# Kernel tuning notes

Hardware: AMD Instinct MI355X
Metric: run time of the kernel (lower is better)

The kernel has to match this reference:

```python
import jax, jax.numpy as jnp
import numpy as np
import math

N, L, E_IN, MDL, H, NE = 8, 4096, 512, 512, 8, 131072
D = MDL // H


def setup_inputs() -> dict:
    key = jax.random.key(0)
    ks = jax.random.split(key, 12)
    s_in = 1.0 / math.sqrt(E_IN)
    s_md = 1.0 / math.sqrt(MDL)
    return {
        "queries": jax.random.normal(ks[0], (N, L, E_IN), jnp.float32),
        "keys": jax.random.normal(ks[1], (N, L, E_IN), jnp.float32),
        "values": jax.random.normal(ks[2], (N, L, E_IN), jnp.float32),
        "adj": jax.random.randint(ks[3], (2, NE), 0, L, jnp.int32),
        "Wq": jax.random.normal(ks[4], (MDL, E_IN), jnp.float32) * s_in,
        "bq": jnp.zeros((MDL,), jnp.float32),
        "Wk": jax.random.normal(ks[5], (MDL, E_IN), jnp.float32) * s_in,
        "bk": jnp.zeros((MDL,), jnp.float32),
        "Wv": jax.random.normal(ks[6], (MDL, E_IN), jnp.float32) * s_in,
        "bv": jnp.zeros((MDL,), jnp.float32),
        "Wfc": jax.random.normal(ks[7], (MDL, MDL), jnp.float32) * s_md,
        "bfc": jnp.zeros((MDL,), jnp.float32),
    }


def _split_head(x):
    n, l, c = x.shape
    return jnp.transpose(x.reshape(n, l, H, c // H), (0, 2, 1, 3))  # (n,h,l,d)


def reference(queries, keys, values, adj, Wq, bq, Wk, bk, Wv, bv, Wfc, bfc):
    q = _split_head(queries @ Wq.T + bq)  # (n,h,l,e)
    k = _split_head(keys @ Wk.T + bk)
    v = _split_head(values @ Wv.T + bv)
    n, h, l, e = q.shape
    temp = 1.0 / math.sqrt(e)
    row, col = adj[0], adj[1]  # query idx / key idx per edge
    # edge-wise QK dot products: (n,h,E)
    qk = temp * jnp.einsum('nhed,nhed->nhe', q[:, :, row, :], k[:, :, col, :])
    # segment softmax over edges grouped by query node (adj[0])
    qk_t = jnp.transpose(qk, (2, 0, 1))  # (E,n,h) - segment ops act on axis 0
    m = jax.ops.segment_max(qk_t, row, num_segments=l)  # (L,n,h)
    ex = jnp.exp(qk_t - m[row])
    den = jax.ops.segment_sum(ex, row, num_segments=l)
    a = ex / den[row]  # (E,n,h); dropout is identity in eval mode
    # spmm: out[i] += a[edge] * v[j] for each edge (i=row, j=col)
    vj = jnp.transpose(v[:, :, col, :], (2, 0, 1, 3))  # (E,n,h,d)
    agg = jax.ops.segment_sum(vj * a[..., None], row, num_segments=l)  # (L,n,h,d)
    out = jnp.transpose(agg, (1, 0, 2, 3)).reshape(n, l, h * e)  # (n,l,h*d)
    return out @ Wfc.T + bfc
```

## Files before the change

kernel.cpp:

```cpp
#include <hip/hip_runtime.h>
#include <cstdint>

typedef __attribute__((ext_vector_type(8))) short short8;
typedef __attribute__((ext_vector_type(8))) _Float16 half8;
typedef __attribute__((ext_vector_type(2))) __fp16 fp16x2;
typedef __attribute__((ext_vector_type(4))) float f32x4;

#define AS1 __attribute__((address_space(1)))
#define AS3 __attribute__((address_space(3)))

constexpr int NB   = 8;
constexpr int L    = 4096;
constexpr int CH   = 512;
constexpr int DD   = 64;
constexpr int NE   = 131072;
constexpr int M_ROWS = NB * L;

template <int CTRL>
__device__ __forceinline__ float dppadd(float s) {
    union { float f; int i; } u, r;
    u.f = s;
    r.i = __builtin_amdgcn_update_dpp(0, u.i, CTRL, 0xF, 0xF, true);
    return s + r.f;
}

__global__ __launch_bounds__(256)
void cvt8_k(const float* __restrict__ src, _Float16* __restrict__ dst) {
    const int i = blockIdx.x * 256 + threadIdx.x;
    const f32x4 a = ((const f32x4*)src)[i * 2];
    const f32x4 b = ((const f32x4*)src)[i * 2 + 1];
    fp16x2 h[4];
    h[0] = __builtin_amdgcn_cvt_pkrtz(a.x, a.y);
    h[1] = __builtin_amdgcn_cvt_pkrtz(a.z, a.w);
    h[2] = __builtin_amdgcn_cvt_pkrtz(b.x, b.y);
    h[3] = __builtin_amdgcn_cvt_pkrtz(b.z, b.w);
    half8 out;
    __builtin_memcpy(&out, h, 16);
    ((half8*)dst)[i] = out;
}

__global__ __launch_bounds__(256)
void cvtw_k(const float* __restrict__ s0, const float* __restrict__ s1,
            const float* __restrict__ s2, const float* __restrict__ s3,
            _Float16* __restrict__ dst) {
    const float* s = (blockIdx.y == 0) ? s0 : (blockIdx.y == 1) ? s1
                   : (blockIdx.y == 2) ? s2 : s3;
    _Float16* d = dst + (size_t)blockIdx.y * (CH * CH);
    const int i = blockIdx.x * 256 + threadIdx.x;
    const f32x4 a = ((const f32x4*)s)[i * 2];
    const f32x4 b = ((const f32x4*)s)[i * 2 + 1];
    fp16x2 h[4];
    h[0] = __builtin_amdgcn_cvt_pkrtz(a.x, a.y);
    h[1] = __builtin_amdgcn_cvt_pkrtz(a.z, a.w);
    h[2] = __builtin_amdgcn_cvt_pkrtz(b.x, b.y);
    h[3] = __builtin_amdgcn_cvt_pkrtz(b.z, b.w);
    half8 out;
    __builtin_memcpy(&out, h, 16);
    ((half8*)d)[i] = out;
}

template <bool OUT_F32>
__global__ __launch_bounds__(256)
void gemm_f16(const _Float16* __restrict__ A, const _Float16* __restrict__ B,
              const float* __restrict__ bias, void* __restrict__ Cp)
{
    __shared__ _Float16 As[128 * 64];
    __shared__ _Float16 Bs[128 * 64];
    const int bid = blockIdx.x;
    const int swz = (bid & 7) * 128 + (bid >> 3);
    const int row0 = (swz >> 2) * 128;
    const int col0 = (swz & 3) * 128;
    const int t = threadIdx.x, lane = t & 63, wid = t >> 6;
    const int wm = (wid >> 1) * 64, wn = (wid & 1) * 64;
    const int fr = lane & 15, fkb = (lane >> 4) * 8;
    const int srow = lane >> 3;
    const int scol = (lane & 7) * 8;

    f32x4 acc[4][4] = {};

    for (int k0 = 0; k0 < CH; k0 += 64) {
#pragma unroll
        for (int q = 0; q < 4; q++) {
            const int r = wid * 32 + q * 8;
            __builtin_amdgcn_global_load_lds(
                (const AS1 unsigned int*)
                    (A + (size_t)(row0 + r + srow) * CH + k0 + scol),
                (AS3 unsigned int*)(As + r * 64), 16, 0, 0);
        }
#pragma unroll
        for (int q = 0; q < 4; q++) {
            const int r = wid * 32 + q * 8;
            __builtin_amdgcn_global_load_lds(
                (const AS1 unsigned int*)
                    (B + (size_t)(col0 + r + srow) * CH + k0 + scol),
                (AS3 unsigned int*)(Bs + r * 64), 16, 0, 0);
        }
        __syncthreads();
#pragma unroll
        for (int kk = 0; kk < 2; kk++) {
            half8 afr[4], bfr[4];
#pragma unroll
            for (int f = 0; f < 4; f++)
                afr[f] = *(const half8*)&As[(wm + f * 16 + fr) * 64 + kk * 32 + fkb];
#pragma unroll
            for (int f = 0; f < 4; f++)
                bfr[f] = *(const half8*)&Bs[(wn + f * 16 + fr) * 64 + kk * 32 + fkb];
#pragma unroll
            for (int fm = 0; fm < 4; fm++)
#pragma unroll
                for (int fn = 0; fn < 4; fn++)
                    acc[fm][fn] = __builtin_amdgcn_mfma_f32_16x16x32_f16(
                        afr[fm], bfr[fn], acc[fm][fn], 0, 0, 0);
        }
        __syncthreads();
    }

    const int rsub = (lane >> 4) * 4;
#pragma unroll
    for (int fn = 0; fn < 4; fn++) {
        const int gc = col0 + wn + fn * 16 + fr;
        const float bv = bias[gc];
#pragma unroll
        for (int fm = 0; fm < 4; fm++) {
            const int gr = row0 + wm + fm * 16 + rsub;
#pragma unroll
            for (int j = 0; j < 4; j++) {
                const float v = acc[fm][fn][j] + bv;
                if constexpr (OUT_F32)
                    ((float*)Cp)[(size_t)(gr + j) * CH + gc] = v;
                else
                    ((_Float16*)Cp)[(size_t)(gr + j) * CH + gc] = (_Float16)v;
            }
        }
    }
}

__global__ void zero_k(int* cnt, int* fill) {
    int i = blockIdx.x * blockDim.x + threadIdx.x;
    if (i < L) { cnt[i] = 0; fill[i] = 0; }
}
__global__ void count_k(const int* __restrict__ adj, int* __restrict__ cnt) {
    int e = blockIdx.x * blockDim.x + threadIdx.x;
    if (e < NE) atomicAdd(&cnt[adj[e]], 1);
}
__global__ void scan_k(const int* __restrict__ cnt, int* __restrict__ rowptr) {
    const int lane = threadIdx.x;
    const int base = lane * 64;
    int s = 0;
    for (int t2 = 0; t2 < 64; t2++) s += cnt[base + t2];
    int incl = s;
    for (int off = 1; off < 64; off <<= 1) {
        int v = __shfl_up(incl, off);
        if (lane >= off) incl += v;
    }
    int run = incl - s;
    for (int t2 = 0; t2 < 64; t2++) { rowptr[base + t2] = run; run += cnt[base + t2]; }
    if (lane == 63) rowptr[L] = run;
}
__global__ void scatter_k(const int* __restrict__ adj, const int* __restrict__ rowptr,
                          int* __restrict__ fill, int* __restrict__ ecol) {
    int e = blockIdx.x * blockDim.x + threadIdx.x;
    if (e < NE) {
        int rr = adj[e];
        int pos = rowptr[rr] + atomicAdd(&fill[rr], 1);
        ecol[pos] = adj[NE + e];
    }
}

__global__ __launch_bounds__(256)
void attn_k(const _Float16* __restrict__ qb, const _Float16* __restrict__ kb,
            const _Float16* __restrict__ vb, const int* __restrict__ rowptr,
            const int* __restrict__ ecol, _Float16* __restrict__ agg)
{
    __shared__ float part[4 * 8 * 65];
    const int bid = blockIdx.x;
    const int n   = bid & 7;
    const int rem = bid >> 3;
    const int hg  = rem >> 12;
    const int i   = rem & 4095;
    const int lane = threadIdx.x & 63;
    const int w    = threadIdx.x >> 6;
    const int h    = hg * 4 + w;
    const int g    = lane & 7;
    const int grp  = lane >> 3;
    const size_t rowbase = ((size_t)(n * L + i)) * CH + h * DD;

    constexpr float SCALE = 0.125f * 1.44269504088896f;
    float qf[8];
    {
        const half8 qu = *(const half8*)(qb + rowbase + g * 8);
#pragma unroll
        for (int e = 0; e < 8; e++) qf[e] = (float)qu[e] * SCALE;
    }
    const int start = rowptr[i], end = rowptr[i + 1];
    const char* kb_g = (const char*)(kb + (size_t)n * L * CH + h * DD) + (g << 4);
    const char* vb_g = (const char*)(vb + (size_t)n * L * CH + h * DD) + (g << 4);

    float o[8] = {};
    float lsum = 0.f;

    const int nIter = (end - start + 7) >> 3;
    int idx = start + grp;
    const int last = end - 1;
    int j0 = (nIter > 0) ? ecol[min(idx, last)] : 0;
    half8 ku = *(const half8*)(kb_g + (j0 << 10));
    half8 vu = *(const half8*)(vb_g + (j0 << 10));
    int j1 = (nIter > 0) ? ecol[min(idx + 8, last)] : 0;

    for (int it = 0; it < nIter; ++it) {
        const half8 kun = *(const half8*)(kb_g + (j1 << 10));
        const half8 vun = *(const half8*)(vb_g + (j1 << 10));
        const int j2 = ecol[min(idx + 16, last)];
        const bool valid = idx < end;
        float s0 = 0.f, s1 = 0.f;
#pragma unroll
        for (int e = 0; e < 4; e++) {
            s0 = fmaf((float)ku[2 * e],     qf[2 * e],     s0);
            s1 = fmaf((float)ku[2 * e + 1], qf[2 * e + 1], s1);
        }
        float s = s0 + s1;
        s = dppadd<0xB1>(s);
        s = dppadd<0x4E>(s);
        s = dppadd<0x141>(s);
        float pe = exp2f(s);
        pe = valid ? pe : 0.f;
#pragma unroll
        for (int e = 0; e < 8; e++)
            o[e] = fmaf((float)vu[e], pe, o[e]);
        lsum += pe;
        ku = kun; vu = vun; j1 = j2; idx += 8;
    }

    lsum += __shfl_xor(lsum, 8);
    lsum += __shfl_xor(lsum, 16);
    lsum += __shfl_xor(lsum, 32);

    float* p = part + w * (8 * 65);
    float* pw = p + grp * 65 + g * 8;
    *(f32x4*)(pw)     = *(f32x4*)&o[0];
    *(f32x4*)(pw + 4) = *(f32x4*)&o[4];
    __builtin_amdgcn_s_waitcnt(0);
    float osum = 0.f;
#pragma unroll
    for (int gg = 0; gg < 8; gg++)
        osum += p[gg * 65 + lane];

    const float inv = (end > start) ? 1.f / lsum : 0.f;
    agg[rowbase + lane] = (_Float16)(osum * inv);
}

extern "C" void kernel_launch(void* const* d_in, const int* in_sizes, int n_in,
                              void* d_out, int out_size, void* d_ws, size_t ws_size,
                              hipStream_t stream)
{
    (void)in_sizes; (void)n_in; (void)out_size; (void)ws_size;
    const float* queries = (const float*)d_in[0];
    const float* keys    = (const float*)d_in[1];
    const float* values  = (const float*)d_in[2];
    const int*   adj     = (const int*)d_in[3];
    const float* Wq  = (const float*)d_in[4];
    const float* bq  = (const float*)d_in[5];
    const float* Wk  = (const float*)d_in[6];
    const float* bk  = (const float*)d_in[7];
    const float* Wv  = (const float*)d_in[8];
    const float* bv  = (const float*)d_in[9];
    const float* Wfc = (const float*)d_in[10];
    const float* bfc = (const float*)d_in[11];

    _Float16* qb = (_Float16*)d_out;
    _Float16* kb = qb + (size_t)M_ROWS * CH;
    uint8_t* w = (uint8_t*)d_ws;
    _Float16* vb  = (_Float16*)(w);
    _Float16* agg = (_Float16*)(w + 33554432);
    _Float16* wf  = (_Float16*)(w + 67108864);
    int* cnt    = (int*)(w + 69206016);
    int* fill   = (int*)(w + 69206016 + 16384);
    int* rowptr = (int*)(w + 69206016 + 32768);
    int* ecol   = (int*)(w + 69206016 + 65536);

    _Float16* stg = agg;
    constexpr int WELEM = CH * CH;

    cvtw_k<<<dim3(WELEM / (256 * 8), 4), 256, 0, stream>>>(Wq, Wk, Wv, Wfc, wf);

    zero_k<<<(L + 255) / 256, 256, 0, stream>>>(cnt, fill);
    count_k<<<(NE + 255) / 256, 256, 0, stream>>>(adj, cnt);
    scan_k<<<1, 64, 0, stream>>>(cnt, rowptr);
    scatter_k<<<(NE + 255) / 256, 256, 0, stream>>>(adj, rowptr, fill, ecol);

    dim3 gg(1024);
    cvt8_k<<<M_ROWS * CH / (256 * 8), 256, 0, stream>>>(queries, stg);
    gemm_f16<false><<<gg, 256, 0, stream>>>(stg, wf + 0 * WELEM, bq, qb);
    cvt8_k<<<M_ROWS * CH / (256 * 8), 256, 0, stream>>>(keys, stg);
    gemm_f16<false><<<gg, 256, 0, stream>>>(stg, wf + 1 * WELEM, bk, kb);
    cvt8_k<<<M_ROWS * CH / (256 * 8), 256, 0, stream>>>(values, stg);
    gemm_f16<false><<<gg, 256, 0, stream>>>(stg, wf + 2 * WELEM, bv, vb);

    attn_k<<<dim3(2 * NB * L), 256, 0, stream>>>(qb, kb, vb, rowptr, ecol, agg);

    gemm_f16<true><<<gg, 256, 0, stream>>>(agg, wf + 3 * WELEM, bfc, (float*)d_out);
}
```

Before: 371.7 us.

## Use packed fp16 dot and accumulation with deeper gather prefetch in edge attention

The per-edge QK dot product now uses packed fp16 fdot2 instead of converting to fp32, and the value accumulation is done in packed half2 FMAs. The K/V gather prefetch is deepened from one to two iterations ahead, and the loop is unrolled by two. The aim is to cut the conversion/ALU work and hide more gather latency. The cost is reduced precision, since the pre-scaled q and the output accumulation are both in fp16, and more registers are held live for the prefetch.

```diff
diff --git a/kernel.cpp b/kernel.cpp
--- a/kernel.cpp
+++ b/kernel.cpp
@@ -3,6 +3,7 @@
 
 typedef __attribute__((ext_vector_type(8))) short short8;
 typedef __attribute__((ext_vector_type(8))) _Float16 half8;
+typedef __attribute__((ext_vector_type(2))) _Float16 h2;
 typedef __attribute__((ext_vector_type(2))) __fp16 fp16x2;
 typedef __attribute__((ext_vector_type(4))) float f32x4;
 
@@ -185,56 +186,87 @@
     const int grp  = lane >> 3;
     const size_t rowbase = ((size_t)(n * L + i)) * CH + h * DD;
 
-    constexpr float SCALE = 0.125f * 1.44269504088896f;
-    float qf[8];
+    fp16x2 qq[4];
     {
         const half8 qu = *(const half8*)(qb + rowbase + g * 8);
-#pragma unroll
-        for (int e = 0; e < 8; e++) qf[e] = (float)qu[e] * SCALE;
+        const _Float16 sc = (_Float16)(0.125f * 1.44269504088896f);
+        h2 qh[4];
+#pragma unroll
+        for (int e = 0; e < 4; e++) {
+            qh[e][0] = qu[2 * e] * sc;
+            qh[e][1] = qu[2 * e + 1] * sc;
+        }
+        __builtin_memcpy(qq, qh, 16);
     }
     const int start = rowptr[i], end = rowptr[i + 1];
-    const char* kb_g = (const char*)(kb + (size_t)n * L * CH + h * DD) + (g << 4);
-    const char* vb_g = (const char*)(vb + (size_t)n * L * CH + h * DD) + (g << 4);
-
-    float o[8] = {};
+    const char* kb_u = (const char*)(kb + (size_t)n * L * CH + h * DD);
+    const char* vb_u = (const char*)(vb + (size_t)n * L * CH + h * DD);
+    const int goff = g << 4;
+
+    h2 o2[4] = {};
     float lsum = 0.f;
 
     const int nIter = (end - start + 7) >> 3;
     int idx = start + grp;
     const int last = end - 1;
-    int j0 = (nIter > 0) ? ecol[min(idx, last)] : 0;
-    half8 ku = *(const half8*)(kb_g + (j0 << 10));
-    half8 vu = *(const half8*)(vb_g + (j0 << 10));
-    int j1 = (nIter > 0) ? ecol[min(idx + 8, last)] : 0;
-
+    half8 k0{}, v0{}, k1{}, v1{};
+    int jC = 0;
+    if (nIter > 0) {
+        const int jA = ecol[min(idx, last)];
+        const int jB = ecol[min(idx + 8, last)];
+        k0 = *(const half8*)(kb_u + ((jA << 10) + goff));
+        v0 = *(const half8*)(vb_u + ((jA << 10) + goff));
+        jC = ecol[min(idx + 16, last)];
+        k1 = *(const half8*)(kb_u + ((jB << 10) + goff));
+        v1 = *(const half8*)(vb_u + ((jB << 10) + goff));
+    }
+
+#pragma unroll 2
     for (int it = 0; it < nIter; ++it) {
-        const half8 kun = *(const half8*)(kb_g + (j1 << 10));
-        const half8 vun = *(const half8*)(vb_g + (j1 << 10));
-        const int j2 = ecol[min(idx + 16, last)];
+        const half8 kn = *(const half8*)(kb_u + ((jC << 10) + goff));
+        const half8 vn = *(const half8*)(vb_u + ((jC << 10) + goff));
+        const int jn = ecol[min(idx + 24, last)];
         const bool valid = idx < end;
-        float s0 = 0.f, s1 = 0.f;
+        fp16x2 kk[4];
+        __builtin_memcpy(kk, &k0, 16);
+        float s = 0.f;
+#if __has_builtin(__builtin_amdgcn_fdot2)
+#pragma unroll
+        for (int e = 0; e < 4; e++)
+            s = __builtin_amdgcn_fdot2(kk[e], qq[e], s, false);
+#else
 #pragma unroll
         for (int e = 0; e < 4; e++) {
-            s0 = fmaf((float)ku[2 * e],     qf[2 * e],     s0);
-            s1 = fmaf((float)ku[2 * e + 1], qf[2 * e + 1], s1);
-        }
-        float s = s0 + s1;
+            s = fmaf((float)kk[e][0], (float)qq[e][0], s);
+            s = fmaf((float)kk[e][1], (float)qq[e][1], s);
+        }
+#endif
         s = dppadd<0xB1>(s);
         s = dppadd<0x4E>(s);
         s = dppadd<0x141>(s);
         float pe = exp2f(s);
         pe = valid ? pe : 0.f;
-#pragma unroll
-        for (int e = 0; e < 8; e++)
-            o[e] = fmaf((float)vu[e], pe, o[e]);
+        const _Float16 ph = (_Float16)pe;
+        const h2 pe2 = {ph, ph};
+        h2 vv[4];
+        __builtin_memcpy(vv, &v0, 16);
+#pragma unroll
+        for (int e = 0; e < 4; e++)
+            o2[e] += pe2 * vv[e];
         lsum += pe;
-        ku = kun; vu = vun; j1 = j2; idx += 8;
+        k0 = k1; v0 = v1; k1 = kn; v1 = vn; jC = jn; idx += 8;
     }
 
     lsum += __shfl_xor(lsum, 8);
     lsum += __shfl_xor(lsum, 16);
     lsum += __shfl_xor(lsum, 32);
 
+    float o[8];
+#pragma unroll
+    for (int e = 0; e < 4; e++) {
+        o[2 * e]     = (float)o2[e][0];
+        o[2 * e + 1] = (float)o2[e][1];
+    }
     float* p = part + w * (8 * 65);
     float* pw = p + grp * 65 + g * 8;
     *(f32x4*)(pw)     = *(f32x4*)&o[0];
```

Measured after the change: 364.7 us. Within noise of the previous version (-1.9%).
